# Optimization experiments

Measured on AMD Instinct MI355X. Metric: run time of the kernel, lower is better.

## Reference

```python
import jax, jax.numpy as jnp
import numpy as np

L = 6          # bandwidth
K = 32         # grid points per Euler angle
B = 8          # batch
CIN = 16
COUT = 32
TOTAL = sum((2 * l + 1) ** 2 for l in range(L))  # 286


def _small_d(beta, order):
    """Small Wigner-d recurrence; beta: [K] -> [K, TOTAL] flattened over (l,m,n)."""
    def off(j):
        return j * (4 * j * j - 1) // 3

    def idx(j, m, mp):
        return off(j) + (2 * j + 1) * (j + m) + j + mp

    W = np.zeros(beta.shape + (TOTAL,))
    cb = np.cos(beta); sb = np.sin(beta)
    cb2 = np.cos(beta * 0.5); sb2 = np.sin(beta * 0.5)
    tb2 = sb2 / cb2
    if order > 0:
        W[..., idx(0, 0, 0)] = 1.0
    if order > 1:
        W[..., idx(1, 0, 0)] = cb
        W[..., idx(1, 1, -1)] = sb2 * sb2
        W[..., idx(1, 1, 0)] = -sb / np.sqrt(2.0)
        W[..., idx(1, 1, 1)] = cb2 * cb2
        W[..., idx(1, 0, 1)] = -W[..., idx(1, 1, 0)]
        W[..., idx(1, 0, -1)] = W[..., idx(1, 1, 0)]
        W[..., idx(1, -1, -1)] = W[..., idx(1, 1, 1)]
        W[..., idx(1, -1, 1)] = W[..., idx(1, 1, -1)]
        W[..., idx(1, -1, 0)] = -W[..., idx(1, 1, 0)]
        d100 = W[..., idx(1, 0, 0)]
        d111 = W[..., idx(1, 1, 1)]
    for i in range(2, order):
        t = i + i - 1
        si = i * i; sim1 = (i - 1) * (i - 1)
        for j in range(i - 1):
            sj = j * j
            for k in range(-j, j + 1):
                sk = k * k
                a = i * t / np.sqrt((si - sj) * (si - sk))
                b = d100 - j * k / (i * (i - 1))
                c = np.sqrt((sim1 - sj) * (sim1 - sk)) / ((i - 1) * t)
                W[..., idx(i, j, k)] = a * (b * W[..., idx(i - 1, j, k)] - c * W[..., idx(i - 2, j, k)])
                W[..., idx(i, k, j)] = (-1) ** (j - k) * W[..., idx(i, j, k)]
                W[..., idx(i, -j, -k)] = (-1) ** (j - k) * W[..., idx(i, j, k)]
                W[..., idx(i, -k, -j)] = W[..., idx(i, j, k)]
        W[..., idx(i, i, i)] = d111 * W[..., idx(i - 1, i - 1, i - 1)]
        W[..., idx(i, -i, -i)] = W[..., idx(i, i, i)]
        W[..., idx(i, i - 1, i - 1)] = (i * d100 - i + 1) * W[..., idx(i - 1, i - 1, i - 1)]
        W[..., idx(i, -i + 1, -i + 1)] = W[..., idx(i, i - 1, i - 1)]
        for mk in range(-i, i):
            k = -mk
            W[..., idx(i, i, k - 1)] = -np.sqrt((i + k) / (i - k + 1)) * tb2 * W[..., idx(i, i, k)]
            W[..., idx(i, k - 1, i)] = (-1) ** (i - k + 1) * W[..., idx(i, i, k - 1)]
            W[..., idx(i, -i, -k + 1)] = (-1) ** (i - k + 1) * W[..., idx(i, i, k - 1)]
            W[..., idx(i, -k + 1, -i)] = W[..., idx(i, i, k - 1)]
        for mk in range(1 - i, i - 1):
            k = -mk
            a = np.sqrt((i + k) / ((i + i) * (i - k + 1)))
            W[..., idx(i, i - 1, k - 1)] = (i * cb - k + 1) * a * W[..., idx(i, i, k)] / d111
            W[..., idx(i, k - 1, i - 1)] = (-1) ** (i - k - 2) * W[..., idx(i, i - 1, k - 1)]
            W[..., idx(i, -i + 1, -k + 1)] = (-1) ** (i - k - 2) * W[..., idx(i, i - 1, k - 1)]
            W[..., idx(i, -k + 1, -i + 1)] = W[..., idx(i, i - 1, k - 1)]
        for k in range(1, i + 1):
            for j in range(k):
                ph = (-1) ** (j + k)
                W[..., idx(i, j, k)] = ph * W[..., idx(i, k, j)]
                W[..., idx(i, j, -k)] = W[..., idx(i, k, -j)]
                W[..., idx(i, -j, k)] = ph * W[..., idx(i, j, -k)]
                W[..., idx(i, -j, -k)] = ph * W[..., idx(i, j, k)]
    return W


def _so3_grid():
    alpha = np.linspace(0, 2 * np.pi, K, endpoint=False)
    x_i = -1 + (np.arange(K) + 0.5) * 2 / K  # 'regular' beta division, w_i = 1
    beta = np.arccos(x_i)
    gamma = np.linspace(0, 2 * np.pi, K, endpoint=False)
    dm = _small_d(beta, L)  # [K, TOTAL]
    inds, fac, mi, ni = [], [], [], []
    for l in range(L):
        for m in range(-l, l + 1):
            for n in range(-l, l + 1):
                if m == 0 and n == 0:
                    fac.append([1, 0, 0, 0])
                elif m == 0 and n > 0:
                    fac.append([np.sqrt(2), 0, 0, 0])
                elif m == 0 and n < 0:
                    fac.append([(-1) ** n * np.sqrt(2), 0, 0, 0])
                elif m > 0 and n == 0:
                    fac.append([np.sqrt(2), 0, 0, 0])
                elif m < 0 and n == 0:
                    fac.append([-(-1) ** m * np.sqrt(2), 0, 0, 0])
                elif m > 0 and n > 0:
                    fac.append([1, (-1) ** n, -1, (-1) ** n])
                elif m > 0 and n < 0:
                    fac.append([(-1) ** n, 1, (-1) ** n, -1])
                elif m < 0 and n > 0:
                    fac.append([-(-1) ** m, -(-1) ** (m + n), -(-1) ** m, (-1) ** (m + n)])
                else:
                    fac.append([-(-1) ** (m + n), -(-1) ** m, (-1) ** (m + n), -(-1) ** m])
                inds.append(l * (4 * l * l - 1) // 3 + (2 * l + 1) * (l + m) + l - n)
                mi.append(m + L - 1)
                ni.append(n + L - 1)
    inds = np.array(inds, dtype=np.int32)
    fac = np.array(fac)
    d1 = fac[:, 0] * dm + fac[:, 1] * dm[:, inds]
    d2 = fac[:, 2] * dm + fac[:, 3] * dm[:, inds]
    ms = np.arange(-L + 1, L)[:, None]  # [2L-1, 1]
    ca1 = np.where(ms < 0, np.sin(ms * alpha), np.cos(ms * alpha))
    ca2 = np.where(ms > 0, np.sin(ms * alpha), np.cos(ms * alpha))
    cg1 = np.where(ms < 0, np.sin(ms * gamma), np.cos(ms * gamma))
    cg2 = np.where(ms > 0, np.sin(ms * gamma), np.cos(ms * gamma))
    return d1, d2, ca1, cg1, ca2, cg2, np.array(mi, np.int32), np.array(ni, np.int32)


def setup_inputs() -> dict:
    key = jax.random.key(0)
    kx, kw = jax.random.split(key)
    d1, d2, ca1, cg1, ca2, cg2, mi, ni = _so3_grid()
    f32 = lambda a: jnp.asarray(a, jnp.float32)
    return {
        "x": jax.random.normal(kx, (B, CIN, TOTAL), jnp.float32),
        "weight": jax.random.normal(kw, (COUT, CIN, TOTAL), jnp.float32) * 0.1,
        "d1": f32(d1), "d2": f32(d2),
        "ca1": f32(ca1), "cg1": f32(cg1), "ca2": f32(ca2), "cg2": f32(cg2),
        "m_idx": jnp.asarray(mi), "n_idx": jnp.asarray(ni),
    }


def reference(x, weight, d1, d2, ca1, cg1, ca2, cg2, m_idx, n_idx):
    # Real Wigner-D grid: Wig[a,b,g,i] = ca1[m_i,a]*d1[b,i]*cg1[n_i,g] + ca2[m_i,a]*d2[b,i]*cg2[n_i,g]
    A1, G1 = ca1[m_idx], cg1[n_idx]  # [TOTAL, K]
    A2, G2 = ca2[m_idx], cg2[n_idx]
    wig = jnp.einsum("ia,bi,ig->abgi", A1, d1, G1) + jnp.einsum("ia,bi,ig->abgi", A2, d2, G2)
    # per-output-channel pattern coefficients, then project onto orientation grid
    y = jnp.einsum("bci,oci->boi", x, weight)              # [B, COUT, TOTAL]
    resp = jnp.einsum("boi,pqri->bopqr", y, wig)           # [B, COUT, K, K, K]
    # orientation-invariant pooling over all rotations
    return resp.max(axis=(2, 3, 4))                         # [B, COUT]
```

## Files before the change

### kernel.cpp

```cpp
#include <hip/hip_runtime.h>

#define TOTAL 286
#define KG 32
#define NM 11
#define CIN 16
#define COUT 32
#define BB 8
#define DROW 16
#define YPN (6 * 16 * DROW)

typedef float    v4f  __attribute__((ext_vector_type(4)));
typedef _Float16 v4h  __attribute__((ext_vector_type(4)));
typedef float    v4fu __attribute__((ext_vector_type(4), aligned(4)));

__global__ __launch_bounds__(1024, 4) void so3_fused(
    const float* __restrict__ x,
    const float* __restrict__ w,
    const float* __restrict__ d1,
    const float* __restrict__ d2,
    const float* __restrict__ ca1,
    const float* __restrict__ cg1,
    const float* __restrict__ ca2,
    const float* __restrict__ cg2,
    float* __restrict__ out)
{
    __shared__ float ySm[288];
    __shared__ __align__(16) float Yp[YPN];
    __shared__ float redw[16];

    const int tid  = threadIdx.x;
    const int lane = tid & 63;
    const int wid  = tid >> 6;
    const int bo   = blockIdx.x;
    const int b    = bo >> 5;
    const int o    = bo & 31;

    if (tid < TOTAL) {
        const float* xp = x + b * CIN * TOTAL + tid;
        const float* wp = w + o * CIN * TOTAL + tid;
        float acc = 0.f;
        #pragma unroll
        for (int c = 0; c < CIN; ++c)
            acc = fmaf(xp[c * TOTAL], wp[c * TOTAL], acc);
        ySm[tid] = acc;
    }

    const int fr = lane & 15;
    const int g  = lane >> 4;
    v4h G1f[2], G2f[2], A1f[2], A2f[2];
    #pragma unroll
    for (int t = 0; t < 2; ++t) {
        #pragma unroll
        for (int i = 0; i < 4; ++i) {
            const int k = 4 * g + i;
            const int c = fr + 16 * t;
            const bool v = (k < NM);
            G1f[t][i] = (_Float16)(v ? cg1[k * KG + c] : 0.f);
            G2f[t][i] = (_Float16)(v ? cg2[k * KG + c] : 0.f);
            A1f[t][i] = (_Float16)(v ? ca1[k * KG + c] : 0.f);
            A2f[t][i] = (_Float16)(v ? ca2[k * KG + c] : 0.f);
        }
    }
    __syncthreads();

    for (int e = tid; e < 6 * 16 * 4; e += 1024) {
        const int gg = e & 3;
        const int m  = (e >> 2) & 15;
        const int l  = e >> 6;
        v4f z = {0.f, 0.f, 0.f, 0.f};
        const int mp = m - 5;
        if (mp >= -l && mp <= l && gg < 3) {
            const int base = l * (4 * l * l - 1) / 3 + (2 * l + 1) * (l + mp) + l - 5;
            #pragma unroll
            for (int j = 0; j < 4; ++j) {
                const int n = 4 * gg + j, np = n - 5;
                if (np >= -l && np <= l) z[j] = ySm[base + n];
            }
        }
        *(v4f*)&Yp[(l * 16 + m) * DROW + 4 * gg] = z;
    }
    __syncthreads();

    v4f ypr[6];
    int dOff[6];
    #pragma unroll
    for (int l = 0; l < 6; ++l) {
        ypr[l] = *(const v4f*)&Yp[(l * 16 + fr) * DROW + 4 * g];
        const int mp = fr - 5;
        const bool valid = (mp >= -l && mp <= l);
        const int base = l * (4 * l * l - 1) / 3 + (2 * l + 1) * (l + mp) + l - 5;
        dOff[l] = valid ? base + 4 * g : 0;
    }

    float lmax = -INFINITY;
    const v4f zero4 = {0.f, 0.f, 0.f, 0.f};

    #pragma unroll
    for (int qi = 0; qi < 2; ++qi) {
        const int q = wid + 16 * qi;
        const float* d1q = d1 + q * TOTAL;
        const float* d2q = d2 + q * TOTAL;

        v4f s1 = zero4, s2 = zero4;
        #pragma unroll
        for (int l = 0; l < 6; ++l) {
            const v4f dv1 = (v4f)(*(const v4fu*)&d1q[dOff[l]]);
            const v4f dv2 = (v4f)(*(const v4fu*)&d2q[dOff[l]]);
            s1 += ypr[l] * dv1;
            s2 += ypr[l] * dv2;
        }
        v4h a1, a2;
        #pragma unroll
        for (int i = 0; i < 4; ++i) { a1[i] = (_Float16)s1[i]; a2[i] = (_Float16)s2[i]; }

        v4f t1a = __builtin_amdgcn_mfma_f32_16x16x16f16(a1, G1f[0], zero4, 0, 0, 0);
        v4f t1b = __builtin_amdgcn_mfma_f32_16x16x16f16(a1, G1f[1], zero4, 0, 0, 0);
        v4f t2a = __builtin_amdgcn_mfma_f32_16x16x16f16(a2, G2f[0], zero4, 0, 0, 0);
        v4f t2b = __builtin_amdgcn_mfma_f32_16x16x16f16(a2, G2f[1], zero4, 0, 0, 0);
        v4h b1a, b1b, b2a, b2b;
        #pragma unroll
        for (int i = 0; i < 4; ++i) {
            b1a[i] = (_Float16)t1a[i]; b1b[i] = (_Float16)t1b[i];
            b2a[i] = (_Float16)t2a[i]; b2b[i] = (_Float16)t2b[i];
        }

        #pragma unroll
        for (int pt = 0; pt < 2; ++pt) {
            v4f acc0 = __builtin_amdgcn_mfma_f32_16x16x16f16(A2f[pt], b2a, zero4, 0, 0, 0);
            acc0     = __builtin_amdgcn_mfma_f32_16x16x16f16(A1f[pt], b1a, acc0, 0, 0, 0);
            v4f acc1 = __builtin_amdgcn_mfma_f32_16x16x16f16(A2f[pt], b2b, zero4, 0, 0, 0);
            acc1     = __builtin_amdgcn_mfma_f32_16x16x16f16(A1f[pt], b1b, acc1, 0, 0, 0);
            #pragma unroll
            for (int j = 0; j < 4; ++j) {
                lmax = fmaxf(lmax, acc0[j]);
                lmax = fmaxf(lmax, acc1[j]);
            }
        }
    }

    #pragma unroll
    for (int off = 32; off > 0; off >>= 1)
        lmax = fmaxf(lmax, __shfl_xor(lmax, off, 64));
    if (lane == 0) redw[wid] = lmax;
    __syncthreads();
    if (tid == 0) {
        float v = redw[0];
        #pragma unroll
        for (int i = 1; i < 16; ++i) v = fmaxf(v, redw[i]);
        out[bo] = v;
    }
}

extern "C" void kernel_launch(void* const* d_in, const int* in_sizes, int n_in,
                              void* d_out, int out_size, void* d_ws, size_t ws_size,
                              hipStream_t stream) {
    const float* x   = (const float*)d_in[0];
    const float* w   = (const float*)d_in[1];
    const float* d1  = (const float*)d_in[2];
    const float* d2  = (const float*)d_in[3];
    const float* ca1 = (const float*)d_in[4];
    const float* cg1 = (const float*)d_in[5];
    const float* ca2 = (const float*)d_in[6];
    const float* cg2 = (const float*)d_in[7];

    so3_fused<<<BB * COUT, 1024, 0, stream>>>(
        x, w, d1, d2, ca1, cg1, ca2, cg2, (float*)d_out);
}
```

Baseline: 13.48 us.

## Split orientation slices across two blocks per output and merge with atomicMax

The grid is doubled so that each (batch, out-channel) pair gets two blocks. Each block handles 16 of the 32 beta slices, one per wave, instead of every wave looping over two. The goal is to use more of the GPU's CUs and shorten the per-block critical path of this small, latency-bound kernel. In exchange, both blocks recompute the channel contraction y. Partial maxima are merged with an integer atomicMax on the float bits, which is only correct for non-negative values and assumes the output buffer starts at a suitable initial value.

```diff
diff --git a/kernel.cpp b/kernel.cpp
--- a/kernel.cpp
+++ b/kernel.cpp
@@ -13,7 +13,7 @@
 typedef _Float16 v4h  __attribute__((ext_vector_type(4)));
 typedef float    v4fu __attribute__((ext_vector_type(4), aligned(4)));
 
-__global__ __launch_bounds__(1024, 4) void so3_fused(
+__global__ __launch_bounds__(1024, 8) void so3_fused(
     const float* __restrict__ x,
     const float* __restrict__ w,
     const float* __restrict__ d1,
@@ -31,9 +31,12 @@
     const int tid  = threadIdx.x;
     const int lane = tid & 63;
     const int wid  = tid >> 6;
-    const int bo   = blockIdx.x;
+    const int gid  = blockIdx.x;
+    const int bo   = gid >> 1;
+    const int half = gid & 1;
     const int b    = bo >> 5;
     const int o    = bo & 31;
+    const int q    = half * 16 + wid;
 
     if (tid < TOTAL) {
         const float* xp = x + b * CIN * TOTAL + tid;
@@ -63,10 +66,10 @@
     }
     __syncthreads();
 
-    for (int e = tid; e < 6 * 16 * 4; e += 1024) {
-        const int gg = e & 3;
-        const int m  = (e >> 2) & 15;
-        const int l  = e >> 6;
+    if (tid < 6 * 16 * 4) {
+        const int gg = tid & 3;
+        const int m  = (tid >> 2) & 15;
+        const int l  = tid >> 6;
         v4f z = {0.f, 0.f, 0.f, 0.f};
         const int mp = m - 5;
         if (mp >= -l && mp <= l && gg < 3) {
@@ -81,60 +84,47 @@
     }
     __syncthreads();
 
-    v4f ypr[6];
-    int dOff[6];
+    const float* d1q = d1 + q * TOTAL;
+    const float* d2q = d2 + q * TOTAL;
+    const v4f zero4 = {0.f, 0.f, 0.f, 0.f};
+
+    v4f s1 = zero4, s2 = zero4;
+    const int mp = fr - 5;
     #pragma unroll
     for (int l = 0; l < 6; ++l) {
-        ypr[l] = *(const v4f*)&Yp[(l * 16 + fr) * DROW + 4 * g];
-        const int mp = fr - 5;
+        const v4f yv = *(const v4f*)&Yp[(l * 16 + fr) * DROW + 4 * g];
         const bool valid = (mp >= -l && mp <= l);
         const int base = l * (4 * l * l - 1) / 3 + (2 * l + 1) * (l + mp) + l - 5;
-        dOff[l] = valid ? base + 4 * g : 0;
+        const int doff = valid ? base + 4 * g : 0;
+        s1 += yv * (v4f)(*(const v4fu*)&d1q[doff]);
+        s2 += yv * (v4f)(*(const v4fu*)&d2q[doff]);
+    }
+    v4h a1, a2;
+    #pragma unroll
+    for (int i = 0; i < 4; ++i) { a1[i] = (_Float16)s1[i]; a2[i] = (_Float16)s2[i]; }
+
+    v4f t1a = __builtin_amdgcn_mfma_f32_16x16x16f16(a1, G1f[0], zero4, 0, 0, 0);
+    v4f t1b = __builtin_amdgcn_mfma_f32_16x16x16f16(a1, G1f[1], zero4, 0, 0, 0);
+    v4f t2a = __builtin_amdgcn_mfma_f32_16x16x16f16(a2, G2f[0], zero4, 0, 0, 0);
+    v4f t2b = __builtin_amdgcn_mfma_f32_16x16x16f16(a2, G2f[1], zero4, 0, 0, 0);
+    v4h b1a, b1b, b2a, b2b;
+    #pragma unroll
+    for (int i = 0; i < 4; ++i) {
+        b1a[i] = (_Float16)t1a[i]; b1b[i] = (_Float16)t1b[i];
+        b2a[i] = (_Float16)t2a[i]; b2b[i] = (_Float16)t2b[i];
     }
 
     float lmax = -INFINITY;
-    const v4f zero4 = {0.f, 0.f, 0.f, 0.f};
-
     #pragma unroll
-    for (int qi = 0; qi < 2; ++qi) {
-        const int q = wid + 16 * qi;
-        const float* d1q = d1 + q * TOTAL;
-        const float* d2q = d2 + q * TOTAL;
-
-        v4f s1 = zero4, s2 = zero4;
+    for (int pt = 0; pt < 2; ++pt) {
+        v4f acc0 = __builtin_amdgcn_mfma_f32_16x16x16f16(A2f[pt], b2a, zero4, 0, 0, 0);
+        acc0     = __builtin_amdgcn_mfma_f32_16x16x16f16(A1f[pt], b1a, acc0, 0, 0, 0);
+        v4f acc1 = __builtin_amdgcn_mfma_f32_16x16x16f16(A2f[pt], b2b, zero4, 0, 0, 0);
+        acc1     = __builtin_amdgcn_mfma_f32_16x16x16f16(A1f[pt], b1b, acc1, 0, 0, 0);
         #pragma unroll
-        for (int l = 0; l < 6; ++l) {
-            const v4f dv1 = (v4f)(*(const v4fu*)&d1q[dOff[l]]);
-            const v4f dv2 = (v4f)(*(const v4fu*)&d2q[dOff[l]]);
-            s1 += ypr[l] * dv1;
-            s2 += ypr[l] * dv2;
-        }
-        v4h a1, a2;
-        #pragma unroll
-        for (int i = 0; i < 4; ++i) { a1[i] = (_Float16)s1[i]; a2[i] = (_Float16)s2[i]; }
-
-        v4f t1a = __builtin_amdgcn_mfma_f32_16x16x16f16(a1, G1f[0], zero4, 0, 0, 0);
-        v4f t1b = __builtin_amdgcn_mfma_f32_16x16x16f16(a1, G1f[1], zero4, 0, 0, 0);
-        v4f t2a = __builtin_amdgcn_mfma_f32_16x16x16f16(a2, G2f[0], zero4, 0, 0, 0);
-        v4f t2b = __builtin_amdgcn_mfma_f32_16x16x16f16(a2, G2f[1], zero4, 0, 0, 0);
-        v4h b1a, b1b, b2a, b2b;
-        #pragma unroll
-        for (int i = 0; i < 4; ++i) {
-            b1a[i] = (_Float16)t1a[i]; b1b[i] = (_Float16)t1b[i];
-            b2a[i] = (_Float16)t2a[i]; b2b[i] = (_Float16)t2b[i];
-        }
-
-        #pragma unroll
-        for (int pt = 0; pt < 2; ++pt) {
-            v4f acc0 = __builtin_amdgcn_mfma_f32_16x16x16f16(A2f[pt], b2a, zero4, 0, 0, 0);
-            acc0     = __builtin_amdgcn_mfma_f32_16x16x16f16(A1f[pt], b1a, acc0, 0, 0, 0);
-            v4f acc1 = __builtin_amdgcn_mfma_f32_16x16x16f16(A2f[pt], b2b, zero4, 0, 0, 0);
-            acc1     = __builtin_amdgcn_mfma_f32_16x16x16f16(A1f[pt], b1b, acc1, 0, 0, 0);
-            #pragma unroll
-            for (int j = 0; j < 4; ++j) {
-                lmax = fmaxf(lmax, acc0[j]);
-                lmax = fmaxf(lmax, acc1[j]);
-            }
+        for (int j = 0; j < 4; ++j) {
+            lmax = fmaxf(lmax, acc0[j]);
+            lmax = fmaxf(lmax, acc1[j]);
         }
     }
 
@@ -147,7 +137,7 @@
         float v = redw[0];
         #pragma unroll
         for (int i = 1; i < 16; ++i) v = fmaxf(v, redw[i]);
-        out[bo] = v;
+        atomicMax((int*)&out[bo], __float_as_int(v));
     }
 }
 
@@ -163,6 +153,6 @@
     const float* ca2 = (const float*)d_in[6];
     const float* cg2 = (const float*)d_in[7];
 
-    so3_fused<<<BB * COUT, 1024, 0, stream>>>(
+    so3_fused<<<BB * COUT * 2, 1024, 0, stream>>>(
         x, w, d1, d2, ca1, cg1, ca2, cg2, (float*)d_out);
 }
```

After: 36.41 us. 2.7x slower.
